# Optimization experiments

Hardware: AMD Instinct MI355X
Metric: run time of the kernel (lower is better)

## Reference

```python
import jax, jax.numpy as jnp
import numpy as np

DIM = 1024
NUM_HEADS = 16
HEAD_DIM = DIM // NUM_HEADS
SCALE = HEAD_DIM ** -0.5


def setup_inputs() -> dict:
    key = jax.random.key(0)
    k1, k2, k3 = jax.random.split(key, 3)
    B, N = 4, 2048
    x = jax.random.normal(k1, (B, N, DIM), dtype=jnp.float32)
    w_qkv = jax.random.normal(k2, (DIM, 3 * DIM), dtype=jnp.float32) * (DIM ** -0.5)
    w_proj = jax.random.normal(k3, (DIM, DIM), dtype=jnp.float32) * (DIM ** -0.5)
    b_proj = jnp.zeros((DIM,), dtype=jnp.float32)
    return {"x": x, "w_qkv": w_qkv, "w_proj": w_proj, "b_proj": b_proj}


def reference(x, w_qkv, w_proj, b_proj):
    B, N, C = x.shape
    H, D = NUM_HEADS, HEAD_DIM
    # qkv projection: (B,N,3C) -> (3,B,H,N,D)
    qkv = (x @ w_qkv).reshape(B, N, 3, H, D).transpose(2, 0, 3, 1, 4)
    q, k, v = qkv[0], qkv[1], qkv[2]
    # full attention scores (B,H,N,N), scaled
    attn = jnp.einsum("bhnd,bhmd->bhnm", q, k) * SCALE
    attn = jax.nn.softmax(attn, axis=-1)
    out = jnp.einsum("bhnm,bhmd->bhnd", attn, v)
    out = out.transpose(0, 2, 1, 3).reshape(B, N, C)
    return out @ w_proj + b_proj
```

## Files before the change

kernel.cpp:

```cpp
#include <hip/hip_runtime.h>
#include <stdint.h>

#define DIM 1024
#define NHEADS 16
#define HDIM 64
#define BATCH 4
#define SEQ 2048
#define NTOK (BATCH*SEQ)
#define SCALE_L2E 0.1803368801111244f

typedef float f32x4 __attribute__((ext_vector_type(4)));
typedef short s16x8 __attribute__((ext_vector_type(8)));

#define MFMA16(a,b,c) __builtin_amdgcn_mfma_f32_16x16x32_bf16((a),(b),(c),0,0,0)

static __device__ __forceinline__ uint16_t f2bf(float f) {
    uint32_t u = __builtin_bit_cast(uint32_t, f);
    return (uint16_t)((u + 0x7FFFu + ((u >> 16) & 1u)) >> 16);
}

static __device__ __forceinline__ uint32_t cvt_pk_bf16(float lo, float hi) {
    uint32_t r;
    asm("v_cvt_pk_bf16_f32 %0, %1, %2" : "=v"(r) : "v"(lo), "v"(hi));
    return r;
}

static __device__ __forceinline__ void gl_lds16(const void* g, void* l) {
    __builtin_amdgcn_global_load_lds(
        (const __attribute__((address_space(1))) unsigned int*)g,
        (__attribute__((address_space(3))) unsigned int*)l, 16, 0, 0);
}

__global__ void convert_f32_bf16(const float* __restrict__ in, uint16_t* __restrict__ out) {
    const int i = blockIdx.x * blockDim.x + threadIdx.x;
    const float4 a = ((const float4*)in)[2*i];
    const float4 b = ((const float4*)in)[2*i + 1];
    ushort4 lo, hi;
    lo.x = f2bf(a.x); lo.y = f2bf(a.y); lo.z = f2bf(a.z); lo.w = f2bf(a.w);
    hi.x = f2bf(b.x); hi.y = f2bf(b.y); hi.z = f2bf(b.z); hi.w = f2bf(b.w);
    ((ushort4*)out)[2*i]     = lo;
    ((ushort4*)out)[2*i + 1] = hi;
}

__global__ void transpose_conv(const float* __restrict__ w, uint16_t* __restrict__ wT,
                               int K, int N) {
    __shared__ float t[32][33];
    const int tx = threadIdx.x, ty = threadIdx.y;
    const int n0 = blockIdx.x * 32, k0 = blockIdx.y * 32;
    #pragma unroll
    for (int i = 0; i < 4; ++i)
        t[ty + i*8][tx] = w[(size_t)(k0 + ty + i*8) * N + n0 + tx];
    __syncthreads();
    #pragma unroll
    for (int i = 0; i < 4; ++i)
        wT[(size_t)(n0 + ty + i*8) * K + k0 + tx] = f2bf(t[tx][ty + i*8]);
}

template <int MODE>
__global__ __launch_bounds__(256) void gemm_bt(
    const uint16_t* __restrict__ A, const uint16_t* __restrict__ B,
    void* __restrict__ C, const float* __restrict__ bias,
    int M, int N, int K)
{
    __shared__ uint16_t As[128*64];
    __shared__ uint16_t Bs[128*64];
    const int tid  = threadIdx.x;
    const int lane = tid & 63;
    const int wid  = tid >> 6;
    const int wm = wid >> 1, wn = wid & 1;
    const long row0 = (long)blockIdx.y * 128;
    const long col0 = (long)blockIdx.x * 128;

    const int sr  = lane >> 3;
    const int scb = (lane & 7) * 16;

    f32x4 acc[4][4] = {};

    for (int kt = 0; kt < K; kt += 64) {
        #pragma unroll
        for (int j = 0; j < 4; ++j) {
            const int r = (wid*4 + j)*8 + sr;
            const int c = (scb ^ ((r & 7) << 4)) >> 1;
            gl_lds16(&A[(row0 + r)*K + kt + c], &As[(wid*4 + j)*512]);
            gl_lds16(&B[(col0 + r)*K + kt + c], &Bs[(wid*4 + j)*512]);
        }
        __syncthreads();
        #pragma unroll
        for (int ks = 0; ks < 2; ++ks) {
            const int xb = (ks*32 + (lane >> 4)*8) * 2;
            s16x8 av[4], bv[4];
            #pragma unroll
            for (int f = 0; f < 4; ++f) {
                const int ra = wm*64 + f*16 + (lane & 15);
                av[f] = *(const s16x8*)((const char*)As + ra*128 + (xb ^ ((ra & 7) << 4)));
                const int rb = wn*64 + f*16 + (lane & 15);
                bv[f] = *(const s16x8*)((const char*)Bs + rb*128 + (xb ^ ((rb & 7) << 4)));
            }
            #pragma unroll
            for (int i = 0; i < 4; ++i)
                #pragma unroll
                for (int j = 0; j < 4; ++j)
                    acc[i][j] = MFMA16(av[i], bv[j], acc[i][j]);
        }
        __syncthreads();
    }

    #pragma unroll
    for (int i = 0; i < 4; ++i) {
        const long row = row0 + wm*64 + i*16 + (lane >> 4)*4;
        #pragma unroll
        for (int j = 0; j < 4; ++j) {
            const long col = col0 + wn*64 + j*16 + (lane & 15);
            #pragma unroll
            for (int r = 0; r < 4; ++r) {
                if (MODE == 0)
                    ((uint16_t*)C)[(row + r)*N + col] = f2bf(acc[i][j][r]);
                else
                    ((float*)C)[(row + r)*N + col] = acc[i][j][r] + bias[col];
            }
        }
    }
}

__global__ __launch_bounds__(256) void gemm_qk(
    const uint16_t* __restrict__ A, const uint16_t* __restrict__ B,
    uint16_t* __restrict__ Qb, uint16_t* __restrict__ Kb)
{
    __shared__ uint16_t As[128*64];
    __shared__ uint16_t Bs[128*64];
    const int K = DIM;
    const int tid  = threadIdx.x;
    const int lane = tid & 63;
    const int wid  = tid >> 6;
    const int wm = wid >> 1, wn = wid & 1;
    const long row0 = (long)blockIdx.y * 128;
    const long col0 = (long)blockIdx.x * 128;

    const int sr  = lane >> 3;
    const int scb = (lane & 7) * 16;

    f32x4 acc[4][4] = {};

    for (int kt = 0; kt < K; kt += 64) {
        #pragma unroll
        for (int j = 0; j < 4; ++j) {
            const int r = (wid*4 + j)*8 + sr;
            const int c = (scb ^ ((r & 7) << 4)) >> 1;
            gl_lds16(&A[(row0 + r)*K + kt + c], &As[(wid*4 + j)*512]);
            gl_lds16(&B[(col0 + r)*K + kt + c], &Bs[(wid*4 + j)*512]);
        }
        __syncthreads();
        #pragma unroll
        for (int ks = 0; ks < 2; ++ks) {
            const int xb = (ks*32 + (lane >> 4)*8) * 2;
            s16x8 av[4], bv[4];
            #pragma unroll
            for (int f = 0; f < 4; ++f) {
                const int ra = wm*64 + f*16 + (lane & 15);
                av[f] = *(const s16x8*)((const char*)As + ra*128 + (xb ^ ((ra & 7) << 4)));
                const int rb = wn*64 + f*16 + (lane & 15);
                bv[f] = *(const s16x8*)((const char*)Bs + rb*128 + (xb ^ ((rb & 7) << 4)));
            }
            #pragma unroll
            for (int i = 0; i < 4; ++i)
                #pragma unroll
                for (int j = 0; j < 4; ++j)
                    acc[i][j] = MFMA16(av[i], bv[j], acc[i][j]);
        }
        __syncthreads();
    }

    #pragma unroll
    for (int i = 0; i < 4; ++i) {
        const int rowl = wm*64 + i*16 + (lane >> 4)*4;
        #pragma unroll
        for (int j = 0; j < 4; ++j) {
            const int col = (int)col0 + wn*64 + j*16 + (lane & 15);
            const int s = col >> 10, h = (col >> 6) & 15, d = col & 63;
            uint16_t* dst = s ? Kb : Qb;
            const float sc = s ? 1.0f : SCALE_L2E;
            #pragma unroll
            for (int r = 0; r < 4; ++r) {
                const long rr = row0 + rowl + r;
                const int b = (int)(rr >> 11), n = (int)(rr & 2047);
                dst[((size_t)(b*NHEADS + h)*SEQ + n)*HDIM + d] = f2bf(acc[i][j][r] * sc);
            }
        }
    }
}

__global__ __launch_bounds__(256) void attn_kernel(
    const uint16_t* __restrict__ Q, const uint16_t* __restrict__ Kg,
    const uint16_t* __restrict__ VT, uint16_t* __restrict__ O)
{
    __shared__ uint16_t Ks[2][64*64];
    __shared__ uint16_t Vs[2][64*64];
    __shared__ uint16_t Ps[128*64];
    const int tid = threadIdx.x, lane = tid & 63, wid = tid >> 6;
    const int qt = blockIdx.x, bh = blockIdx.y;
    const int b = bh >> 4, h = bh & 15;
    const uint16_t* Qh = Q  + (size_t)bh * SEQ * HDIM;
    const uint16_t* Kh = Kg + (size_t)bh * SEQ * HDIM;
    const uint16_t* Vh = VT + (size_t)h * HDIM * NTOK + (size_t)b * SEQ;
    const int qbase = qt*128 + wid*32;
    const int g = lane >> 4, q15 = lane & 15;
    const int swl = (lane & 7) << 4;

    s16x8 bq[2][2];
    #pragma unroll
    for (int i = 0; i < 2; ++i)
        #pragma unroll
        for (int ks = 0; ks < 2; ++ks)
            bq[i][ks] = *(const s16x8*)&Qh[(size_t)(qbase + i*16 + q15)*HDIM + ks*32 + g*8];

    f32x4 o[2][4] = {};
    f32x4 lacc[2] = {};

    const int sr  = lane >> 3;
    const int scb = (lane & 7) * 16;
    const int stg_c = (scb ^ ((sr) << 4)) >> 1;

    #define STAGE(bf, t)                                                          \
        _Pragma("unroll")                                                         \
        for (int j = 0; j < 2; ++j) {                                             \
            const int r = (wid*2 + j)*8 + sr;                                     \
            gl_lds16(&Kh[(size_t)((t)*64 + r)*HDIM + stg_c], &Ks[bf][(wid*2 + j)*512]); \
            gl_lds16(&Vh[(size_t)r*NTOK + (t)*64 + stg_c],   &Vs[bf][(wid*2 + j)*512]); \
        }

    STAGE(0, 0)
    __syncthreads();

    for (int it = 0; it < 32; ++it) {
        const int cur = it & 1;
        if (it < 31) STAGE(cur ^ 1, it + 1)

        const uint16_t* ksb = Ks[cur];
        const uint16_t* vsb = Vs[cur];

        f32x4 st[2][4] = {};
        #pragma unroll
        for (int ks = 0; ks < 2; ++ks) {
            const int xb = (ks*32 + g*8) * 2;
            s16x8 ak[4];
            #pragma unroll
            for (int f = 0; f < 4; ++f) {
                const int rk = f*16 + q15;
                ak[f] = *(const s16x8*)((const char*)ksb + rk*128 + (xb ^ ((rk & 7) << 4)));
            }
            #pragma unroll
            for (int i = 0; i < 2; ++i)
                #pragma unroll
                for (int f = 0; f < 4; ++f)
                    st[i][f] = MFMA16(ak[f], bq[i][ks], st[i][f]);
        }

        #pragma unroll
        for (int i = 0; i < 2; ++i) {
            #pragma unroll
            for (int f = 0; f < 4; ++f) {
                #pragma unroll
                for (int r = 0; r < 4; ++r)
                    st[i][f][r] = __builtin_amdgcn_exp2f(st[i][f][r]);
            }
            lacc[i] += (st[i][0] + st[i][1]) + (st[i][2] + st[i][3]);
        }

        #pragma unroll
        for (int i = 0; i < 2; ++i) {
            char* base = (char*)Ps + (wid*32 + i*16 + q15)*128;
            #pragma unroll
            for (int f = 0; f < 4; ++f) {
                uint2 w;
                w.x = cvt_pk_bf16(st[i][f][0], st[i][f][1]);
                w.y = cvt_pk_bf16(st[i][f][2], st[i][f][3]);
                *(uint2*)(base + ((f*32 + g*8) ^ swl)) = w;
            }
        }

        #pragma unroll
        for (int ks = 0; ks < 2; ++ks) {
            s16x8 pa[2], vb[4];
            #pragma unroll
            for (int i = 0; i < 2; ++i)
                pa[i] = *(const s16x8*)((const char*)Ps + (wid*32 + i*16 + q15)*128
                                         + ((ks*64 + g*16) ^ swl));
            const int xbv = (ks*32 + g*8) * 2;
            #pragma unroll
            for (int f = 0; f < 4; ++f) {
                const int rv = f*16 + q15;
                vb[f] = *(const s16x8*)((const char*)vsb + rv*128 + (xbv ^ ((rv & 7) << 4)));
            }
            #pragma unroll
            for (int i = 0; i < 2; ++i)
                #pragma unroll
                for (int f = 0; f < 4; ++f)
                    o[i][f] = MFMA16(pa[i], vb[f], o[i][f]);
        }

        __syncthreads();
    }
    #undef STAGE

    #pragma unroll
    for (int i = 0; i < 2; ++i) {
        float ls = (lacc[i][0] + lacc[i][1]) + (lacc[i][2] + lacc[i][3]);
        ls += __shfl_xor(ls, 16);
        ls += __shfl_xor(ls, 32);
        #pragma unroll
        for (int r = 0; r < 4; ++r) {
            const float l_r = __shfl(ls, g*4 + r);
            const float inv = 1.0f / l_r;
            const int n = qbase + i*16 + g*4 + r;
            const size_t base = ((size_t)b*SEQ + n)*DIM + h*HDIM;
            #pragma unroll
            for (int f = 0; f < 4; ++f)
                O[base + f*16 + q15] = f2bf(o[i][f][r] * inv);
        }
    }
}

extern "C" void kernel_launch(void* const* d_in, const int* in_sizes, int n_in,
                              void* d_out, int out_size, void* d_ws, size_t ws_size,
                              hipStream_t stream)
{
    const float* x      = (const float*)d_in[0];
    const float* w_qkv  = (const float*)d_in[1];
    const float* w_proj = (const float*)d_in[2];
    const float* b_proj = (const float*)d_in[3];
    float* out = (float*)d_out;

    uint16_t* xb     = (uint16_t*)d_ws;
    uint16_t* wqkvT  = xb     + (size_t)NTOK*DIM;
    uint16_t* wprojT = wqkvT  + (size_t)3*DIM*DIM;
    uint16_t* Qb     = wprojT + (size_t)DIM*DIM;
    uint16_t* Kb     = Qb     + (size_t)NTOK*DIM;
    uint16_t* VTb    = Kb     + (size_t)NTOK*DIM;
    uint16_t* attn_o = VTb    + (size_t)NTOK*DIM;

    convert_f32_bf16<<<dim3(NTOK*DIM/8/256), dim3(256), 0, stream>>>(x, xb);
    transpose_conv<<<dim3(96, 32), dim3(32, 8), 0, stream>>>(w_qkv, wqkvT, DIM, 3*DIM);
    transpose_conv<<<dim3(32, 32), dim3(32, 8), 0, stream>>>(w_proj, wprojT, DIM, DIM);
    gemm_qk<<<dim3(16, 64), dim3(256), 0, stream>>>(xb, wqkvT, Qb, Kb);
    gemm_bt<0><<<dim3(64, 8), dim3(256), 0, stream>>>(wqkvT + (size_t)2*DIM*DIM, xb,
                                                      VTb, nullptr, DIM, NTOK, DIM);
    attn_kernel<<<dim3(16, 64), dim3(256), 0, stream>>>(Qb, Kb, VTb, attn_o);
    gemm_bt<1><<<dim3(8, 64), dim3(256), 0, stream>>>(attn_o, wprojT, out, b_proj, NTOK, DIM, DIM);
}
```

Baseline: 209.1 us.

## Switch attention to 32x32 MFMA and keep P in registers via permlane swap

Rewrites the attention inner loop to use 32x32x16 bf16 MFMA tiles, with each wave covering 32 query rows. The softmax probabilities are repacked in registers with v_permlane32_swap so they feed the PV MFMA directly, which removes the LDS round-trip for P along with its shared buffer. The output epilogue writes packed 32-bit bf16 pairs and drops the per-row shuffles. The exp and normalisation maths are unchanged, but the register layout and swizzled LDS indexing change, so correctness depends on the new operand mapping being right.

Measured after the change: 215.9 us. 3.3% more time.

```diff
diff --git a/kernel.cpp b/kernel.cpp
--- a/kernel.cpp
+++ b/kernel.cpp
@@ -9,10 +9,12 @@
 #define NTOK (BATCH*SEQ)
 #define SCALE_L2E 0.1803368801111244f
 
-typedef float f32x4 __attribute__((ext_vector_type(4)));
-typedef short s16x8 __attribute__((ext_vector_type(8)));
+typedef float f32x4  __attribute__((ext_vector_type(4)));
+typedef float f32x16 __attribute__((ext_vector_type(16)));
+typedef short s16x8  __attribute__((ext_vector_type(8)));
 
 #define MFMA16(a,b,c) __builtin_amdgcn_mfma_f32_16x16x32_bf16((a),(b),(c),0,0,0)
+#define MFMA32(a,b,c) __builtin_amdgcn_mfma_f32_32x32x16_bf16((a),(b),(c),0,0,0)
 
 static __device__ __forceinline__ uint16_t f2bf(float f) {
     uint32_t u = __builtin_bit_cast(uint32_t, f);
@@ -195,7 +197,6 @@
 {
     __shared__ uint16_t Ks[2][64*64];
     __shared__ uint16_t Vs[2][64*64];
-    __shared__ uint16_t Ps[128*64];
     const int tid = threadIdx.x, lane = tid & 63, wid = tid >> 6;
     const int qt = blockIdx.x, bh = blockIdx.y;
     const int b = bh >> 4, h = bh & 15;
@@ -203,22 +204,19 @@
     const uint16_t* Kh = Kg + (size_t)bh * SEQ * HDIM;
     const uint16_t* Vh = VT + (size_t)h * HDIM * NTOK + (size_t)b * SEQ;
     const int qbase = qt*128 + wid*32;
-    const int g = lane >> 4, q15 = lane & 15;
-    const int swl = (lane & 7) << 4;
-
-    s16x8 bq[2][2];
-    #pragma unroll
-    for (int i = 0; i < 2; ++i)
-        #pragma unroll
-        for (int ks = 0; ks < 2; ++ks)
-            bq[i][ks] = *(const s16x8*)&Qh[(size_t)(qbase + i*16 + q15)*HDIM + ks*32 + g*8];
-
-    f32x4 o[2][4] = {};
-    f32x4 lacc[2] = {};
+    const int q31 = lane & 31, half = lane >> 5;
+
+    s16x8 bq[4];
+    #pragma unroll
+    for (int ks = 0; ks < 4; ++ks)
+        bq[ks] = *(const s16x8*)&Qh[(size_t)(qbase + q31)*HDIM + ks*16 + half*8];
+
+    f32x16 o0 = {}, o1 = {};
+    float lsum = 0.f;
 
     const int sr  = lane >> 3;
     const int scb = (lane & 7) * 16;
-    const int stg_c = (scb ^ ((sr) << 4)) >> 1;
+    const int stg_c = (scb ^ (sr << 4)) >> 1;
 
     #define STAGE(bf, t)                                                          \
         _Pragma("unroll")                                                         \
@@ -231,91 +229,83 @@
     STAGE(0, 0)
     __syncthreads();
 
+    const int swz = (q31 & 7) << 4;
+    const int rb0 = q31 * 128;
+
     for (int it = 0; it < 32; ++it) {
         const int cur = it & 1;
         if (it < 31) STAGE(cur ^ 1, it + 1)
 
-        const uint16_t* ksb = Ks[cur];
-        const uint16_t* vsb = Vs[cur];
-
-        f32x4 st[2][4] = {};
-        #pragma unroll
-        for (int ks = 0; ks < 2; ++ks) {
-            const int xb = (ks*32 + g*8) * 2;
-            s16x8 ak[4];
-            #pragma unroll
-            for (int f = 0; f < 4; ++f) {
-                const int rk = f*16 + q15;
-                ak[f] = *(const s16x8*)((const char*)ksb + rk*128 + (xb ^ ((rk & 7) << 4)));
-            }
-            #pragma unroll
-            for (int i = 0; i < 2; ++i)
-                #pragma unroll
-                for (int f = 0; f < 4; ++f)
-                    st[i][f] = MFMA16(ak[f], bq[i][ks], st[i][f]);
-        }
-
-        #pragma unroll
-        for (int i = 0; i < 2; ++i) {
-            #pragma unroll
-            for (int f = 0; f < 4; ++f) {
-                #pragma unroll
-                for (int r = 0; r < 4; ++r)
-                    st[i][f][r] = __builtin_amdgcn_exp2f(st[i][f][r]);
-            }
-            lacc[i] += (st[i][0] + st[i][1]) + (st[i][2] + st[i][3]);
-        }
-
-        #pragma unroll
-        for (int i = 0; i < 2; ++i) {
-            char* base = (char*)Ps + (wid*32 + i*16 + q15)*128;
-            #pragma unroll
-            for (int f = 0; f < 4; ++f) {
-                uint2 w;
-                w.x = cvt_pk_bf16(st[i][f][0], st[i][f][1]);
-                w.y = cvt_pk_bf16(st[i][f][2], st[i][f][3]);
-                *(uint2*)(base + ((f*32 + g*8) ^ swl)) = w;
-            }
-        }
-
-        #pragma unroll
-        for (int ks = 0; ks < 2; ++ks) {
-            s16x8 pa[2], vb[4];
-            #pragma unroll
-            for (int i = 0; i < 2; ++i)
-                pa[i] = *(const s16x8*)((const char*)Ps + (wid*32 + i*16 + q15)*128
-                                         + ((ks*64 + g*16) ^ swl));
-            const int xbv = (ks*32 + g*8) * 2;
-            #pragma unroll
-            for (int f = 0; f < 4; ++f) {
-                const int rv = f*16 + q15;
-                vb[f] = *(const s16x8*)((const char*)vsb + rv*128 + (xbv ^ ((rv & 7) << 4)));
-            }
-            #pragma unroll
-            for (int i = 0; i < 2; ++i)
-                #pragma unroll
-                for (int f = 0; f < 4; ++f)
-                    o[i][f] = MFMA16(pa[i], vb[f], o[i][f]);
+        const char* ksb = (const char*)Ks[cur];
+        const char* vsb = (const char*)Vs[cur];
+
+        f32x16 st0 = {}, st1 = {};
+        #pragma unroll
+        for (int ks = 0; ks < 4; ++ks) {
+            const int xb = ((ks*32 + half*16) ^ swz);
+            const s16x8 k0 = *(const s16x8*)(ksb + rb0 + xb);
+            const s16x8 k1 = *(const s16x8*)(ksb + rb0 + 4096 + xb);
+            st0 = MFMA32(k0, bq[ks], st0);
+            st1 = MFMA32(k1, bq[ks], st1);
+        }
+
+        #pragma unroll
+        for (int r = 0; r < 16; ++r) {
+            st0[r] = __builtin_amdgcn_exp2f(st0[r]);
+            st1[r] = __builtin_amdgcn_exp2f(st1[r]);
+        }
+        {
+            f32x16 ts = st0 + st1;
+            float a0 = (ts[0]+ts[1]) + (ts[2]+ts[3]);
+            float a1 = (ts[4]+ts[5]) + (ts[6]+ts[7]);
+            float a2 = (ts[8]+ts[9]) + (ts[10]+ts[11]);
+            float a3 = (ts[12]+ts[13]) + (ts[14]+ts[15]);
+            lsum += (a0+a1) + (a2+a3);
+        }
+
+        #pragma unroll
+        for (int t = 0; t < 2; ++t) {
+            const f32x16 stt = t ? st1 : st0;
+            uint32_t pk_[8];
+            #pragma unroll
+            for (int m = 0; m < 4; ++m) {
+                pk_[2*m]   = cvt_pk_bf16(stt[4*m+0], stt[4*m+1]);
+                pk_[2*m+1] = cvt_pk_bf16(stt[4*m+2], stt[4*m+3]);
+            }
+            #pragma unroll
+            for (int sl = 0; sl < 2; ++sl) {
+                uint32_t u0 = pk_[4*sl+0], u1 = pk_[4*sl+1];
+                uint32_t u2 = pk_[4*sl+2], u3 = pk_[4*sl+3];
+                asm("v_permlane32_swap_b32 %0, %1" : "+v"(u0), "+v"(u2));
+                asm("v_permlane32_swap_b32 %0, %1" : "+v"(u1), "+v"(u3));
+                union { uint32_t u[4]; s16x8 v; } pf = {{u0, u1, u2, u3}};
+                const int s = t*2 + sl;
+                const int xb = ((s*16 + half*8)*2) ^ swz;
+                const s16x8 v0 = *(const s16x8*)(vsb + rb0 + xb);
+                const s16x8 v1 = *(const s16x8*)(vsb + rb0 + 4096 + xb);
+                o0 = MFMA32(v0, pf.v, o0);
+                o1 = MFMA32(v1, pf.v, o1);
+            }
         }
 
         __syncthreads();
     }
     #undef STAGE
 
-    #pragma unroll
-    for (int i = 0; i < 2; ++i) {
-        float ls = (lacc[i][0] + lacc[i][1]) + (lacc[i][2] + lacc[i][3]);
-        ls += __shfl_xor(ls, 16);
-        ls += __shfl_xor(ls, 32);
-        #pragma unroll
-        for (int r = 0; r < 4; ++r) {
-            const float l_r = __shfl(ls, g*4 + r);
-            const float inv = 1.0f / l_r;
-            const int n = qbase + i*16 + g*4 + r;
-            const size_t base = ((size_t)b*SEQ + n)*DIM + h*HDIM;
-            #pragma unroll
-            for (int f = 0; f < 4; ++f)
-                O[base + f*16 + q15] = f2bf(o[i][f][r] * inv);
+    const float ls  = lsum + __shfl_xor(lsum, 32);
+    const float inv = 1.0f / ls;
+    const int n = qbase + q31;
+    uint16_t* outp = O + ((size_t)b*SEQ + n)*DIM + h*HDIM;
+    #pragma unroll
+    for (int dt = 0; dt < 2; ++dt) {
+        const f32x16 ot = dt ? o1 : o0;
+        #pragma unroll
+        for (int m = 0; m < 4; ++m) {
+            const int d0 = dt*32 + 8*m + 4*half;
+            const uint32_t w0 = cvt_pk_bf16(ot[4*m+0]*inv, ot[4*m+1]*inv);
+            const uint32_t w1 = cvt_pk_bf16(ot[4*m+2]*inv, ot[4*m+3]*inv);
+            *(uint32_t*)(outp + d0)     = w0;
+            *(uint32_t*)(outp + d0 + 2) = w1;
         }
     }
 }
```

## Software-pipeline attention loop: overlap next QK^T with current softmax and PV

Applied to the files above, without the earlier changes.

Restructures the attention KV loop into a two-stage software pipeline. The QK^T MFMAs for tile t+1 are issued alongside the exp/P-store/PV of tile t, and K and V staging are split so K runs one tile ahead of V. The aim is to hide the dependent exp and LDS round-trip latency behind independent MFMA work. In exchange it doubles the score accumulator registers (stA/stB), which may raise VGPR pressure and lower occupancy.

Result: slower. 213.5 us (+2.1%).

```diff
diff --git a/kernel.cpp b/kernel.cpp
--- a/kernel.cpp
+++ b/kernel.cpp
@@ -9,8 +9,8 @@
 #define NTOK (BATCH*SEQ)
 #define SCALE_L2E 0.1803368801111244f
 
-typedef float f32x4 __attribute__((ext_vector_type(4)));
-typedef short s16x8 __attribute__((ext_vector_type(8)));
+typedef float f32x4  __attribute__((ext_vector_type(4)));
+typedef short s16x8  __attribute__((ext_vector_type(8)));
 
 #define MFMA16(a,b,c) __builtin_amdgcn_mfma_f32_16x16x32_bf16((a),(b),(c),0,0,0)
 
@@ -205,6 +205,7 @@
     const int qbase = qt*128 + wid*32;
     const int g = lane >> 4, q15 = lane & 15;
     const int swl = (lane & 7) << 4;
+    const f32x4 fzero = {};
 
     s16x8 bq[2][2];
     #pragma unroll
@@ -215,92 +216,127 @@
 
     f32x4 o[2][4] = {};
     f32x4 lacc[2] = {};
+    f32x4 stA[2][4], stB[2][4];
 
     const int sr  = lane >> 3;
     const int scb = (lane & 7) * 16;
-    const int stg_c = (scb ^ ((sr) << 4)) >> 1;
-
-    #define STAGE(bf, t)                                                          \
-        _Pragma("unroll")                                                         \
-        for (int j = 0; j < 2; ++j) {                                             \
-            const int r = (wid*2 + j)*8 + sr;                                     \
-            gl_lds16(&Kh[(size_t)((t)*64 + r)*HDIM + stg_c], &Ks[bf][(wid*2 + j)*512]); \
-            gl_lds16(&Vh[(size_t)r*NTOK + (t)*64 + stg_c],   &Vs[bf][(wid*2 + j)*512]); \
-        }
-
-    STAGE(0, 0)
+    const int stg_c = (scb ^ (sr << 4)) >> 1;
+
+#define STAGE_K(bf_, t_) do {                                                     \
+    _Pragma("unroll")                                                             \
+    for (int j_ = 0; j_ < 2; ++j_) {                                              \
+        const int r_ = (wid*2 + j_)*8 + sr;                                       \
+        gl_lds16(&Kh[(size_t)((t_)*64 + r_)*HDIM + stg_c], &Ks[bf_][(wid*2 + j_)*512]); \
+    }                                                                             \
+} while (0)
+
+#define STAGE_V(bf_, t_) do {                                                     \
+    _Pragma("unroll")                                                             \
+    for (int j_ = 0; j_ < 2; ++j_) {                                              \
+        const int r_ = (wid*2 + j_)*8 + sr;                                       \
+        gl_lds16(&Vh[(size_t)r_*NTOK + (t_)*64 + stg_c], &Vs[bf_][(wid*2 + j_)*512]); \
+    }                                                                             \
+} while (0)
+
+#define QKT(ST_, t_) do {                                                         \
+    const char* ksb_ = (const char*)Ks[(t_)&1];                                   \
+    _Pragma("unroll")                                                             \
+    for (int i_ = 0; i_ < 2; ++i_)                                                \
+        _Pragma("unroll")                                                         \
+        for (int f_ = 0; f_ < 4; ++f_) ST_[i_][f_] = fzero;                       \
+    _Pragma("unroll")                                                             \
+    for (int ks_ = 0; ks_ < 2; ++ks_) {                                           \
+        const int xb_ = (ks_*32 + g*8) * 2;                                       \
+        s16x8 ak_[4];                                                             \
+        _Pragma("unroll")                                                         \
+        for (int f_ = 0; f_ < 4; ++f_) {                                          \
+            const int rk_ = f_*16 + q15;                                          \
+            ak_[f_] = *(const s16x8*)(ksb_ + rk_*128 + (xb_ ^ ((rk_ & 7) << 4))); \
+        }                                                                         \
+        _Pragma("unroll")                                                         \
+        for (int i_ = 0; i_ < 2; ++i_)                                            \
+            _Pragma("unroll")                                                     \
+            for (int f_ = 0; f_ < 4; ++f_)                                        \
+                ST_[i_][f_] = MFMA16(ak_[f_], bq[i_][ks_], ST_[i_][f_]);          \
+    }                                                                             \
+} while (0)
+
+#define SOFTPV(ST_, t_) do {                                                      \
+    const char* vsb_ = (const char*)Vs[(t_)&1];                                   \
+    _Pragma("unroll")                                                             \
+    for (int i_ = 0; i_ < 2; ++i_) {                                              \
+        _Pragma("unroll")                                                         \
+        for (int f_ = 0; f_ < 4; ++f_)                                            \
+            _Pragma("unroll")                                                     \
+            for (int r_ = 0; r_ < 4; ++r_)                                        \
+                ST_[i_][f_][r_] = __builtin_amdgcn_exp2f(ST_[i_][f_][r_]);        \
+        lacc[i_] += (ST_[i_][0] + ST_[i_][1]) + (ST_[i_][2] + ST_[i_][3]);        \
+    }                                                                             \
+    _Pragma("unroll")                                                             \
+    for (int i_ = 0; i_ < 2; ++i_) {                                              \
+        char* pb_ = (char*)Ps + (wid*32 + i_*16 + q15)*128;                       \
+        _Pragma("unroll")                                                         \
+        for (int f_ = 0; f_ < 4; ++f_) {                                          \
+            uint2 w_;                                                             \
+            w_.x = cvt_pk_bf16(ST_[i_][f_][0], ST_[i_][f_][1]);                   \
+            w_.y = cvt_pk_bf16(ST_[i_][f_][2], ST_[i_][f_][3]);                   \
+            *(uint2*)(pb_ + ((f_*32 + g*8) ^ swl)) = w_;                          \
+        }                                                                         \
+    }                                                                             \
+    _Pragma("unroll")                                                             \
+    for (int ks_ = 0; ks_ < 2; ++ks_) {                                           \
+        s16x8 pa_[2], vb_[4];                                                     \
+        _Pragma("unroll")                                                         \
+        for (int i_ = 0; i_ < 2; ++i_)                                            \
+            pa_[i_] = *(const s16x8*)((const char*)Ps + (wid*32 + i_*16 + q15)*128 \
+                                      + ((ks_*64 + g*16) ^ swl));                 \
+        const int xbv_ = (ks_*32 + g*8) * 2;                                      \
+        _Pragma("unroll")                                                         \
+        for (int f_ = 0; f_ < 4; ++f_) {                                          \
+            const int rv_ = f_*16 + q15;                                          \
+            vb_[f_] = *(const s16x8*)(vsb_ + rv_*128 + (xbv_ ^ ((rv_ & 7) << 4))); \
+        }                                                                         \
+        _Pragma("unroll")                                                         \
+        for (int i_ = 0; i_ < 2; ++i_)                                            \
+            _Pragma("unroll")                                                     \
+            for (int f_ = 0; f_ < 4; ++f_)                                        \
+                o[i_][f_] = MFMA16(pa_[i_], vb_[f_], o[i_][f_]);                  \
+    }                                                                             \
+} while (0)
+
+    STAGE_K(0, 0);
     __syncthreads();
 
-    for (int it = 0; it < 32; ++it) {
-        const int cur = it & 1;
-        if (it < 31) STAGE(cur ^ 1, it + 1)
-
-        const uint16_t* ksb = Ks[cur];
-        const uint16_t* vsb = Vs[cur];
-
-        f32x4 st[2][4] = {};
-        #pragma unroll
-        for (int ks = 0; ks < 2; ++ks) {
-            const int xb = (ks*32 + g*8) * 2;
-            s16x8 ak[4];
-            #pragma unroll
-            for (int f = 0; f < 4; ++f) {
-                const int rk = f*16 + q15;
-                ak[f] = *(const s16x8*)((const char*)ksb + rk*128 + (xb ^ ((rk & 7) << 4)));
-            }
-            #pragma unroll
-            for (int i = 0; i < 2; ++i)
-                #pragma unroll
-                for (int f = 0; f < 4; ++f)
-                    st[i][f] = MFMA16(ak[f], bq[i][ks], st[i][f]);
-        }
-
-        #pragma unroll
-        for (int i = 0; i < 2; ++i) {
-            #pragma unroll
-            for (int f = 0; f < 4; ++f) {
-                #pragma unroll
-                for (int r = 0; r < 4; ++r)
-                    st[i][f][r] = __builtin_amdgcn_exp2f(st[i][f][r]);
-            }
-            lacc[i] += (st[i][0] + st[i][1]) + (st[i][2] + st[i][3]);
-        }
-
-        #pragma unroll
-        for (int i = 0; i < 2; ++i) {
-            char* base = (char*)Ps + (wid*32 + i*16 + q15)*128;
-            #pragma unroll
-            for (int f = 0; f < 4; ++f) {
-                uint2 w;
-                w.x = cvt_pk_bf16(st[i][f][0], st[i][f][1]);
-                w.y = cvt_pk_bf16(st[i][f][2], st[i][f][3]);
-                *(uint2*)(base + ((f*32 + g*8) ^ swl)) = w;
-            }
-        }
-
-        #pragma unroll
-        for (int ks = 0; ks < 2; ++ks) {
-            s16x8 pa[2], vb[4];
-            #pragma unroll
-            for (int i = 0; i < 2; ++i)
-                pa[i] = *(const s16x8*)((const char*)Ps + (wid*32 + i*16 + q15)*128
-                                         + ((ks*64 + g*16) ^ swl));
-            const int xbv = (ks*32 + g*8) * 2;
-            #pragma unroll
-            for (int f = 0; f < 4; ++f) {
-                const int rv = f*16 + q15;
-                vb[f] = *(const s16x8*)((const char*)vsb + rv*128 + (xbv ^ ((rv & 7) << 4)));
-            }
-            #pragma unroll
-            for (int i = 0; i < 2; ++i)
-                #pragma unroll
-                for (int f = 0; f < 4; ++f)
-                    o[i][f] = MFMA16(pa[i], vb[f], o[i][f]);
-        }
-
-        __syncthreads();
-    }
-    #undef STAGE
+    STAGE_K(1, 1);
+    STAGE_V(0, 0);
+    QKT(stA, 0);
+    __syncthreads();
+
+    for (int tt = 0; tt < 15; ++tt) {
+        const int t1 = 2*tt + 1, t2 = 2*tt + 2;
+        STAGE_K(0, t1 + 1);
+        STAGE_V(1, t1);
+        QKT(stB, t1);
+        SOFTPV(stA, t1 - 1);
+        __syncthreads();
+        STAGE_K(1, t2 + 1);
+        STAGE_V(0, t2);
+        QKT(stA, t2);
+        SOFTPV(stB, t2 - 1);
+        __syncthreads();
+    }
+
+    STAGE_V(1, 31);
+    QKT(stB, 31);
+    SOFTPV(stA, 30);
+    __syncthreads();
+
+    SOFTPV(stB, 31);
+
+#undef STAGE_K
+#undef STAGE_V
+#undef QKT
+#undef SOFTPV
 
     #pragma unroll
     for (int i = 0; i < 2; ++i) {
```

## Fuse Q/K/V projections into one double-buffered 256x192-tile GEMM with setprio

Applied to the files above, without the earlier changes.

Replaces the separate Q/K GEMM and V-transpose GEMM with a single QKV GEMM. It uses 512-thread blocks, a 256x192 output tile, double-buffered LDS and a swizzled block order, and writes V transposed straight from the accumulators. This removes one launch and reloading x twice, and raises per-block reuse. It also adds s_setprio around the MFMA bursts in all GEMMs and in attention so other waves can issue loads. The larger LDS footprint (about 112KB) and register use may limit occupancy, and the V store stride is uncoalesced per lane.

Result: slower. 215.0 us (+2.8%).

```diff
diff --git a/kernel.cpp b/kernel.cpp
--- a/kernel.cpp
+++ b/kernel.cpp
@@ -9,8 +9,8 @@
 #define NTOK (BATCH*SEQ)
 #define SCALE_L2E 0.1803368801111244f
 
-typedef float f32x4 __attribute__((ext_vector_type(4)));
-typedef short s16x8 __attribute__((ext_vector_type(8)));
+typedef float f32x4  __attribute__((ext_vector_type(4)));
+typedef short s16x8  __attribute__((ext_vector_type(8)));
 
 #define MFMA16(a,b,c) __builtin_amdgcn_mfma_f32_16x16x32_bf16((a),(b),(c),0,0,0)
 
@@ -96,11 +96,13 @@
                 const int rb = wn*64 + f*16 + (lane & 15);
                 bv[f] = *(const s16x8*)((const char*)Bs + rb*128 + (xb ^ ((rb & 7) << 4)));
             }
+            __builtin_amdgcn_s_setprio(1);
             #pragma unroll
             for (int i = 0; i < 4; ++i)
                 #pragma unroll
                 for (int j = 0; j < 4; ++j)
                     acc[i][j] = MFMA16(av[i], bv[j], acc[i][j]);
+            __builtin_amdgcn_s_setprio(0);
         }
         __syncthreads();
     }
@@ -122,68 +124,95 @@
     }
 }
 
-__global__ __launch_bounds__(256) void gemm_qk(
+__global__ __launch_bounds__(512, 2) void qkv_gemm(
     const uint16_t* __restrict__ A, const uint16_t* __restrict__ B,
-    uint16_t* __restrict__ Qb, uint16_t* __restrict__ Kb)
+    uint16_t* __restrict__ Qb, uint16_t* __restrict__ Kb,
+    uint16_t* __restrict__ VTb)
 {
-    __shared__ uint16_t As[128*64];
-    __shared__ uint16_t Bs[128*64];
-    const int K = DIM;
-    const int tid  = threadIdx.x;
-    const int lane = tid & 63;
-    const int wid  = tid >> 6;
-    const int wm = wid >> 1, wn = wid & 1;
-    const long row0 = (long)blockIdx.y * 128;
-    const long col0 = (long)blockIdx.x * 128;
-
-    const int sr  = lane >> 3;
-    const int scb = (lane & 7) * 16;
-
-    f32x4 acc[4][4] = {};
-
-    for (int kt = 0; kt < K; kt += 64) {
-        #pragma unroll
-        for (int j = 0; j < 4; ++j) {
-            const int r = (wid*4 + j)*8 + sr;
-            const int c = (scb ^ ((r & 7) << 4)) >> 1;
-            gl_lds16(&A[(row0 + r)*K + kt + c], &As[(wid*4 + j)*512]);
-            gl_lds16(&B[(col0 + r)*K + kt + c], &Bs[(wid*4 + j)*512]);
-        }
+    __shared__ uint16_t As[2][256*64];
+    __shared__ uint16_t Bs[2][192*64];
+    const int tid = threadIdx.x, lane = tid & 63, wid = tid >> 6;
+    const int wr = wid >> 2, wc = wid & 3;
+    const int q15 = lane & 15, g = lane >> 4;
+
+    int bid = blockIdx.y * gridDim.x + blockIdx.x;
+    bid = (bid & 7) * 64 + (bid >> 3);
+    const int  bx  = bid & 15;
+    const long row0 = (long)(bid >> 4) * 256;
+    const int  col0 = bx * 192;
+
+    const int r_  = tid >> 3;
+    const int sc  = (((tid & 7) * 16) ^ ((r_ & 7) << 4)) >> 1;
+
+    f32x4 acc[8][3] = {};
+
+#define QSTAGE(bf_, t_) do {                                                    \
+    const int kt_ = (t_) * 64;                                                  \
+    _Pragma("unroll")                                                           \
+    for (int j_ = 0; j_ < 4; ++j_)                                              \
+        gl_lds16(&A[(row0 + j_*64 + r_)*DIM + kt_ + sc], &As[bf_][j_*4096 + tid*8]); \
+    _Pragma("unroll")                                                           \
+    for (int j_ = 0; j_ < 3; ++j_)                                              \
+        gl_lds16(&B[(size_t)(col0 + j_*64 + r_)*DIM + kt_ + sc], &Bs[bf_][j_*4096 + tid*8]); \
+} while (0)
+
+    QSTAGE(0, 0);
+
+    for (int t = 0; t < 16; ++t) {
+        const int p = t & 1;
         __syncthreads();
+        QSTAGE(p ^ 1, (t < 15 ? t + 1 : 15));
         #pragma unroll
         for (int ks = 0; ks < 2; ++ks) {
-            const int xb = (ks*32 + (lane >> 4)*8) * 2;
-            s16x8 av[4], bv[4];
-            #pragma unroll
-            for (int f = 0; f < 4; ++f) {
-                const int ra = wm*64 + f*16 + (lane & 15);
-                av[f] = *(const s16x8*)((const char*)As + ra*128 + (xb ^ ((ra & 7) << 4)));
-                const int rb = wn*64 + f*16 + (lane & 15);
-                bv[f] = *(const s16x8*)((const char*)Bs + rb*128 + (xb ^ ((rb & 7) << 4)));
-            }
-            #pragma unroll
-            for (int i = 0; i < 4; ++i)
-                #pragma unroll
-                for (int j = 0; j < 4; ++j)
-                    acc[i][j] = MFMA16(av[i], bv[j], acc[i][j]);
-        }
-        __syncthreads();
-    }
-
-    #pragma unroll
-    for (int i = 0; i < 4; ++i) {
-        const int rowl = wm*64 + i*16 + (lane >> 4)*4;
-        #pragma unroll
-        for (int j = 0; j < 4; ++j) {
-            const int col = (int)col0 + wn*64 + j*16 + (lane & 15);
-            const int s = col >> 10, h = (col >> 6) & 15, d = col & 63;
+            const int xb = (ks*32 + g*8) * 2;
+            s16x8 av[8], bv[3];
+            #pragma unroll
+            for (int m = 0; m < 8; ++m) {
+                const int ra = wr*128 + m*16 + q15;
+                av[m] = *(const s16x8*)((const char*)As[p] + ra*128 + (xb ^ ((ra & 7) << 4)));
+            }
+            #pragma unroll
+            for (int n = 0; n < 3; ++n) {
+                const int rb = wc*48 + n*16 + q15;
+                bv[n] = *(const s16x8*)((const char*)Bs[p] + rb*128 + (xb ^ ((rb & 7) << 4)));
+            }
+            __builtin_amdgcn_s_setprio(1);
+            #pragma unroll
+            for (int m = 0; m < 8; ++m)
+                #pragma unroll
+                for (int n = 0; n < 3; ++n)
+                    acc[m][n] = MFMA16(av[m], bv[n], acc[m][n]);
+            __builtin_amdgcn_s_setprio(0);
+        }
+    }
+#undef QSTAGE
+
+    #pragma unroll
+    for (int n = 0; n < 3; ++n) {
+        const int c = col0 + wc*48 + n*16 + q15;
+        const int s = c >> 10;
+        if (s == 2) {
+            const int vrow = c - 2048;
+            #pragma unroll
+            for (int m = 0; m < 8; ++m) {
+                const long rr = row0 + wr*128 + m*16 + g*4;
+                uint2 w;
+                w.x = cvt_pk_bf16(acc[m][n][0], acc[m][n][1]);
+                w.y = cvt_pk_bf16(acc[m][n][2], acc[m][n][3]);
+                *(uint2*)&VTb[(size_t)vrow*NTOK + rr] = w;
+            }
+        } else {
             uint16_t* dst = s ? Kb : Qb;
-            const float sc = s ? 1.0f : SCALE_L2E;
-            #pragma unroll
-            for (int r = 0; r < 4; ++r) {
-                const long rr = row0 + rowl + r;
-                const int b = (int)(rr >> 11), n = (int)(rr & 2047);
-                dst[((size_t)(b*NHEADS + h)*SEQ + n)*HDIM + d] = f2bf(acc[i][j][r] * sc);
+            const float scl = s ? 1.0f : SCALE_L2E;
+            const int hd = (c >> 6) & 15, d = c & 63;
+            #pragma unroll
+            for (int m = 0; m < 8; ++m) {
+                #pragma unroll
+                for (int r = 0; r < 4; ++r) {
+                    const long rr = row0 + wr*128 + m*16 + g*4 + r;
+                    const int b = (int)(rr >> 11), nt = (int)(rr & 2047);
+                    dst[((size_t)(b*NHEADS + hd)*SEQ + nt)*HDIM + d] = f2bf(acc[m][n][r] * scl);
+                }
             }
         }
     }
@@ -218,7 +247,7 @@
 
     const int sr  = lane >> 3;
     const int scb = (lane & 7) * 16;
-    const int stg_c = (scb ^ ((sr) << 4)) >> 1;
+    const int stg_c = (scb ^ (sr << 4)) >> 1;
 
     #define STAGE(bf, t)                                                          \
         _Pragma("unroll")                                                         \
@@ -235,8 +264,8 @@
         const int cur = it & 1;
         if (it < 31) STAGE(cur ^ 1, it + 1)
 
-        const uint16_t* ksb = Ks[cur];
-        const uint16_t* vsb = Vs[cur];
+        const char* ksb = (const char*)Ks[cur];
+        const char* vsb = (const char*)Vs[cur];
 
         f32x4 st[2][4] = {};
         #pragma unroll
@@ -246,13 +275,15 @@
             #pragma unroll
             for (int f = 0; f < 4; ++f) {
                 const int rk = f*16 + q15;
-                ak[f] = *(const s16x8*)((const char*)ksb + rk*128 + (xb ^ ((rk & 7) << 4)));
-            }
+                ak[f] = *(const s16x8*)(ksb + rk*128 + (xb ^ ((rk & 7) << 4)));
+            }
+            __builtin_amdgcn_s_setprio(1);
             #pragma unroll
             for (int i = 0; i < 2; ++i)
                 #pragma unroll
                 for (int f = 0; f < 4; ++f)
                     st[i][f] = MFMA16(ak[f], bq[i][ks], st[i][f]);
+            __builtin_amdgcn_s_setprio(0);
         }
 
         #pragma unroll
@@ -289,13 +320,15 @@
             #pragma unroll
             for (int f = 0; f < 4; ++f) {
                 const int rv = f*16 + q15;
-                vb[f] = *(const s16x8*)((const char*)vsb + rv*128 + (xbv ^ ((rv & 7) << 4)));
-            }
+                vb[f] = *(const s16x8*)(vsb + rv*128 + (xbv ^ ((rv & 7) << 4)));
+            }
+            __builtin_amdgcn_s_setprio(1);
             #pragma unroll
             for (int i = 0; i < 2; ++i)
                 #pragma unroll
                 for (int f = 0; f < 4; ++f)
                     o[i][f] = MFMA16(pa[i], vb[f], o[i][f]);
+            __builtin_amdgcn_s_setprio(0);
         }
 
         __syncthreads();
@@ -341,9 +374,7 @@
     convert_f32_bf16<<<dim3(NTOK*DIM/8/256), dim3(256), 0, stream>>>(x, xb);
     transpose_conv<<<dim3(96, 32), dim3(32, 8), 0, stream>>>(w_qkv, wqkvT, DIM, 3*DIM);
     transpose_conv<<<dim3(32, 32), dim3(32, 8), 0, stream>>>(w_proj, wprojT, DIM, DIM);
-    gemm_qk<<<dim3(16, 64), dim3(256), 0, stream>>>(xb, wqkvT, Qb, Kb);
-    gemm_bt<0><<<dim3(64, 8), dim3(256), 0, stream>>>(wqkvT + (size_t)2*DIM*DIM, xb,
-                                                      VTb, nullptr, DIM, NTOK, DIM);
+    qkv_gemm<<<dim3(16, 32), dim3(512), 0, stream>>>(xb, wqkvT, Qb, Kb, VTb);
     attn_kernel<<<dim3(16, 64), dim3(256), 0, stream>>>(Qb, Kb, VTb, attn_o);
     gemm_bt<1><<<dim3(8, 64), dim3(256), 0, stream>>>(attn_o, wprojT, out, b_proj, NTOK, DIM, DIM);
 }
```
